# Optimization experiments

Measured on AMD Instinct MI355X. Metric: run time of the kernel, lower is better.

Reference implementation:

```python
import jax, jax.numpy as jnp
import numpy as np

M, N, K, D_IN = 200, 6, 25, 784
GAMMA, EPS = 0.5, 0.5
TOTAL = M * N


def setup_inputs() -> dict:
    key = jax.random.key(0)
    ks = jax.random.split(key, 8)
    B = 16384
    def lin(kk, shape, fan_in):
        bound = 1.0 / np.sqrt(fan_in)
        return jax.random.uniform(kk, shape, jnp.float32, -bound, bound)
    return {
        "batch_x": jax.random.normal(ks[0], (B, D_IN), jnp.float32),
        "Wa": lin(ks[1], (M, D_IN), D_IN),
        "ba": lin(ks[2], (M,), D_IN),
        "Wb": lin(ks[3], (TOTAL, TOTAL), TOTAL),
        "bb": lin(ks[4], (TOTAL,), TOTAL),
        "Wd": lin(ks[5], (D_IN, M), M),
        "bd": lin(ks[6], (D_IN,), M),
    }


def _step(params, carry, x):
    Wa, ba, Wb, bb, Wd, bd = params
    x_b, phi, psi = carry
    # sigma: per-group drive broadcast over cells + full recurrent term, shape (m, n)
    z_a = (Wa @ x + ba)[:, None]                      # (m, 1)
    z_b = (Wb @ x_b + bb).reshape(M, N)               # (m, n)
    sigma = z_a + z_b
    # inhibited activity
    pi = (1.0 - phi) * (sigma - sigma.min() + 1.0)    # (m, n)
    lambda_i = pi.max(axis=1)                         # (m,)
    # top-1 cell per group (scatter of topk indices == one-hot argmax)
    M_pi = jax.nn.one_hot(jnp.argmax(pi, axis=1), N, dtype=sigma.dtype)
    # top-k groups
    _, idx = jax.lax.top_k(lambda_i, K)
    M_lambda = jnp.zeros((M,), sigma.dtype).at[idx].set(1.0)[:, None]
    y = jnp.tanh(M_pi * M_lambda * sigma)             # (m, n)
    x_a_pred = Wd @ y.max(axis=1) + bd                # (D_in,)
    # memory / inhibition updates
    psi_n = jnp.maximum(EPS * psi, y)
    phi_n = jnp.maximum(GAMMA * phi, y)
    alpha = psi_n.sum()
    alpha = jnp.where(alpha == 0.0, 1.0, alpha)
    x_b_n = (psi_n / alpha).reshape(-1)
    # original detaches the recurrent state each step
    carry_n = (jax.lax.stop_gradient(x_b_n),
               jax.lax.stop_gradient(phi_n),
               jax.lax.stop_gradient(psi_n))
    return carry_n, x_a_pred


def reference(batch_x, Wa, ba, Wb, bb, Wd, bd):
    params = (Wa, ba, Wb, bb, Wd, bd)
    carry0 = (jnp.zeros((TOTAL,), batch_x.dtype),
              jnp.zeros((M, N), batch_x.dtype),
              jnp.zeros((M, N), batch_x.dtype))
    (x_b, phi, psi), preds = jax.lax.scan(
        lambda c, x: _step(params, c, x), carry0, batch_x)
    return preds, x_b, phi, psi
```

## Files before the change

### kernel.cpp

```cpp
#include <hip/hip_runtime.h>
#include <math.h>

#define Tn   16384
#define Mg   200
#define Nc   6
#define TOT  1200
#define Kk   25
#define Din  784
#define SP   28

__global__ void transpose_k(const float* __restrict__ src, float* __restrict__ dst,
                            int R, int C) {
    __shared__ float tile[32][33];
    int bx = blockIdx.x * 32, by = blockIdx.y * 32;
    int x = bx + threadIdx.x;
    for (int j = 0; j < 32; j += 8) {
        int y = by + threadIdx.y + j;
        if (x < C && y < R) tile[threadIdx.y + j][threadIdx.x] = src[(size_t)y * C + x];
    }
    __syncthreads();
    int x2 = by + threadIdx.x;
    for (int j = 0; j < 32; j += 8) {
        int y2 = bx + threadIdx.y + j;
        if (x2 < R && y2 < C) dst[(size_t)y2 * R + x2] = tile[threadIdx.x][threadIdx.y + j];
    }
}

__global__ void za_k(const float* __restrict__ X, const float* __restrict__ Wa,
                     const float* __restrict__ ba, float* __restrict__ Za) {
    __shared__ float xs[16][788];
    const int tid = threadIdx.x;
    const int t0  = blockIdx.x * 16;
    for (int idx = tid; idx < 16 * Din; idx += 256) {
        int tt = idx / Din, kk = idx - tt * Din;
        xs[tt][kk] = X[(size_t)(t0 + tt) * Din + kk];
    }
    __syncthreads();
    const int tq = tid & 15, gq = tid >> 4;
    const float4* xrow = reinterpret_cast<const float4*>(&xs[tq][0]);
    for (int g = gq; g < Mg; g += 16) {
        float acc = ba[g];
        const float4* wrow = reinterpret_cast<const float4*>(Wa + (size_t)g * Din);
        for (int k4 = 0; k4 < Din / 4; ++k4) {
            float4 a = xrow[k4], b = wrow[k4];
            acc = fmaf(a.x, b.x, acc); acc = fmaf(a.y, b.y, acc);
            acc = fmaf(a.z, b.z, acc); acc = fmaf(a.w, b.w, acc);
        }
        Za[(size_t)(t0 + tq) * Mg + g] = acc;
    }
}

__launch_bounds__(384, 1)
__global__ void serial_k(const float* __restrict__ Za, const float* __restrict__ WbT,
                         const float* __restrict__ bb,
                         unsigned long long* __restrict__ YP,
                         float* __restrict__ outTail) {
    __shared__ alignas(16) float sigma_sh[50 * SP];
    __shared__ alignas(16) float minp[8];
    __shared__ alignas(16) float selD[32];
    __shared__ alignas(16) int   selO[32];
    __shared__ float alphaS;

    const int tid  = threadIdx.x;
    const int lane = tid & 63;

    if (tid < 64) {
        const bool grp = (lane < 50);
        const int sgb  = lane * SP;
        const int cell0 = 24 * lane;
        const unsigned long long lt = (1ull << lane) - 1ull;

        float ps[24];
        #pragma unroll
        for (int i = 0; i < 24; ++i) ps[i] = 0.f;
        unsigned long long thw = 0ull;
        int slotr[4] = {-1, -1, -1, -1};
        unsigned long long yv64[4] = {0ull, 0ull, 0ull, 0ull};
        int bj[4] = {0, 0, 0, 0};
        float dcl[4] = {0.f, 0.f, 0.f, 0.f};

        __syncthreads();

        for (int t = 0; t < Tn; ++t) {
            if (t > 0) {
                #pragma unroll
                for (int c = 0; c < 4; ++c)
                    if (slotr[c] >= 0) YP[(size_t)(t - 1) * Kk + slotr[c]] = yv64[c];
            }

            float4 mp4 = *reinterpret_cast<const float4*>(minp);
            float m = fminf(fminf(fminf(mp4.x, mp4.y), fminf(mp4.z, mp4.w)), minp[4]);
            const float m1 = 1.f - m;

            float sg[24];
            if (grp) {
                #pragma unroll
                for (int q = 0; q < 6; ++q) {
                    float4 v = *reinterpret_cast<const float4*>(sigma_sh + sgb + 4 * q);
                    sg[4*q] = v.x; sg[4*q+1] = v.y; sg[4*q+2] = v.z; sg[4*q+3] = v.w;
                }
            } else {
                #pragma unroll
                for (int i = 0; i < 24; ++i) sg[i] = 0.f;
            }

            float bs[4], bp[4]; unsigned long long kb[4];
            #pragma unroll
            for (int c = 0; c < 4; ++c) { bs[c]=0.f; bp[c]=0.f; bj[c]=0; kb[c]=0ull; }
            if (grp) {
                #pragma unroll
                for (int c = 0; c < 4; ++c) {
                    float best = -INFINITY, sbv = 0.f, pbv = 0.f; int jb = 0;
                    #pragma unroll
                    for (int j = 0; j < 6; ++j) {
                        int i = 6 * c + j;
                        float pv = (1.f - ps[i]) * (sg[i] + m1);
                        bool bet = pv > best;
                        best = bet ? pv : best;
                        jb  = bet ? j : jb;
                        sbv = bet ? sg[i] : sbv;
                        pbv = bet ? ps[i] : pbv;
                    }
                    unsigned ub = __float_as_uint(best);
                    ub ^= (unsigned)(((int)ub) >> 31) | 0x80000000u;
                    int g = 4 * lane + c;
                    kb[c] = ((unsigned long long)ub << 32) |
                            (unsigned long long)(0xFFFFFFFFu - (unsigned)g);
                    bs[c] = sbv; bp[c] = pbv; bj[c] = jb;
                }
            }

            unsigned long long A = 0ull, B = ~0ull;
            unsigned long long p = thw;
            unsigned long long theta;
            while (true) {
                int cnt = __popcll(__ballot(kb[0] >= p)) + __popcll(__ballot(kb[1] >= p))
                        + __popcll(__ballot(kb[2] >= p)) + __popcll(__ballot(kb[3] >= p));
                if (cnt == Kk) { theta = p; break; }
                if (cnt > Kk) A = p; else B = p;
                unsigned long long m0 = __ballot(kb[0] > A && kb[0] < B);
                unsigned long long m1b = __ballot(kb[1] > A && kb[1] < B);
                unsigned long long m2 = __ballot(kb[2] > A && kb[2] < B);
                unsigned long long m3 = __ballot(kb[3] > A && kb[3] < B);
                int cls; unsigned long long mm;
                if (m0)       { cls = 0; mm = m0; }
                else if (m1b) { cls = 1; mm = m1b; }
                else if (m2)  { cls = 2; mm = m2; }
                else          { cls = 3; mm = m3; }
                int sl = __ffsll(mm) - 1;
                unsigned long long kc = (cls==0)?kb[0]:(cls==1)?kb[1]:(cls==2)?kb[2]:kb[3];
                p = __shfl(kc, sl);
            }
            thw = theta;

            unsigned long long M0 = __ballot(kb[0] >= theta);
            unsigned long long M1 = __ballot(kb[1] >= theta);
            unsigned long long M2 = __ballot(kb[2] >= theta);
            unsigned long long M3 = __ballot(kb[3] >= theta);
            int base1 = __popcll(M0);
            int base2 = base1 + __popcll(M1);
            int base3 = base2 + __popcll(M2);

            #pragma unroll
            for (int c = 0; c < 4; ++c) {
                slotr[c] = -1;
                unsigned long long Mc = (c==0)?M0:(c==1)?M1:(c==2)?M2:M3;
                int bse = (c==0)?0:(c==1)?base1:(c==2)?base2:base3;
                bool s = grp && (kb[c] >= theta);
                float d = 0.f;
                if (s) {
                    int slot = bse + __popcll(Mc & lt);
                    float x = fminf(fmaxf(bs[c], -9.f), 9.f);
                    float e = __expf(2.f * x);
                    float y = 1.f - 2.f / (e + 1.f);
                    float yv = fmaxf(y, 0.f);
                    d = fmaxf(y - 0.5f * bp[c], 0.f);
                    int g = 4 * lane + c;
                    selD[slot] = d;
                    selO[slot] = (6 * g + bj[c]) * TOT;
                    slotr[c] = slot;
                    yv64[c] = ((unsigned long long)(unsigned)g << 32) |
                              (unsigned long long)__float_as_uint(yv);
                }
                dcl[c] = d;
            }

            __syncthreads();

            if (grp) {
                #pragma unroll
                for (int c = 0; c < 4; ++c) {
                    #pragma unroll
                    for (int j = 0; j < 6; ++j) {
                        int i = 6 * c + j;
                        float add = (j == bj[c]) ? dcl[c] : 0.f;
                        ps[i] = fmaf(ps[i], 0.5f, add);
                    }
                }
            }

            __syncthreads();
        }

        #pragma unroll
        for (int c = 0; c < 4; ++c)
            if (slotr[c] >= 0) YP[(size_t)(Tn - 1) * Kk + slotr[c]] = yv64[c];
        if (grp) {
            float a = alphaS;
            float inv2 = (a == 0.f) ? 1.f : (1.f / a);
            #pragma unroll
            for (int i = 0; i < 24; ++i) {
                outTail[cell0 + i]           = ps[i] * inv2;
                outTail[TOT + cell0 + i]     = ps[i];
                outTail[2 * TOT + cell0 + i] = ps[i];
            }
        }
    } else {
        const int j = tid - 64;
        const bool act = (j < 300);
        const int w = (tid >> 6) - 1;
        const int base = act ? 4 * j : 0;
        const int saddr = act ? ((j / 6) * SP + (4 * j) % 24) : 0;
        const int g0 = base / 6, g1 = (base + 3) / 6;
        const bool f1 = ((base + 1) / 6) != g0;
        const bool f2 = ((base + 2) / 6) != g0;
        const bool f3 = ((base + 3) / 6) != g0;

        float4 cb4 = make_float4(0.f, 0.f, 0.f, 0.f);
        if (act) cb4 = *reinterpret_cast<const float4*>(bb + base);
        float4 uo = make_float4(0.f, 0.f, 0.f, 0.f);
        float alpha = 0.f;

        {
            float za0 = act ? Za[g0] : 0.f;
            float za1 = act ? Za[g1] : 0.f;
            float s0 = cb4.x + za0;
            float s1 = cb4.y + (f1 ? za1 : za0);
            float s2 = cb4.z + (f2 ? za1 : za0);
            float s3 = cb4.w + (f3 ? za1 : za0);
            if (act)
                *reinterpret_cast<float4*>(sigma_sh + saddr) = make_float4(s0,s1,s2,s3);
            float lm = act ? fminf(fminf(s0, s1), fminf(s2, s3)) : INFINITY;
            #pragma unroll
            for (int o = 1; o < 64; o <<= 1) lm = fminf(lm, __shfl_xor(lm, o));
            if (lane == 0) minp[w] = lm;
        }
        __syncthreads();

        for (int t = 0; t < Tn; ++t) {
            uo.x *= 0.5f; uo.y *= 0.5f; uo.z *= 0.5f; uo.w *= 0.5f;

            __syncthreads();

            float vD = 0.f; int vO = 0;
            if (lane < 25) { vD = selD[lane]; vO = selO[lane]; }

            const int tn = (t + 1 < Tn) ? t + 1 : t;
            float nza0 = act ? Za[(size_t)tn * Mg + g0] : 0.f;
            float nza1 = act ? Za[(size_t)tn * Mg + g1] : 0.f;
            float4 cc[Kk];
            #pragma unroll
            for (int k = 0; k < Kk; ++k) {
                int offk = __builtin_amdgcn_readlane(vO, k);
                cc[k] = *reinterpret_cast<const float4*>(WbT + offk + base);
            }
            __builtin_amdgcn_sched_barrier(0);

            float av = vD;
            #pragma unroll
            for (int o = 1; o < 64; o <<= 1) av += __shfl_xor(av, o);
            alpha = fmaf(alpha, 0.5f, av);
            const float A0  = (alpha == 0.f) ? 1.f : alpha;
            const float inv = 1.f / A0;
            if (w == 0 && lane == 0) alphaS = alpha;

            #pragma unroll
            for (int k = 0; k < Kk; ++k) {
                float dk = __uint_as_float(
                    (unsigned)__builtin_amdgcn_readlane((int)__float_as_uint(vD), k));
                uo.x = fmaf(dk, cc[k].x, uo.x);
                uo.y = fmaf(dk, cc[k].y, uo.y);
                uo.z = fmaf(dk, cc[k].z, uo.z);
                uo.w = fmaf(dk, cc[k].w, uo.w);
            }

            float s0 = fmaf(uo.x, inv, cb4.x + nza0);
            float s1 = fmaf(uo.y, inv, cb4.y + (f1 ? nza1 : nza0));
            float s2 = fmaf(uo.z, inv, cb4.z + (f2 ? nza1 : nza0));
            float s3 = fmaf(uo.w, inv, cb4.w + (f3 ? nza1 : nza0));
            if (act)
                *reinterpret_cast<float4*>(sigma_sh + saddr) = make_float4(s0,s1,s2,s3);
            float lm = act ? fminf(fminf(s0, s1), fminf(s2, s3)) : INFINITY;
            #pragma unroll
            for (int o = 1; o < 64; o <<= 1) lm = fminf(lm, __shfl_xor(lm, o));
            if (lane == 0) minp[w] = lm;

            __syncthreads();
        }
    }
}

__global__ void preds_k(const unsigned long long* __restrict__ YP,
                        const float* __restrict__ WdT, const float* __restrict__ bd,
                        float* __restrict__ out) {
    const int t = blockIdx.x;
    __shared__ float sv[Kk];
    __shared__ int   si[Kk];
    if (threadIdx.x < Kk) {
        unsigned long long v = YP[(size_t)t * Kk + threadIdx.x];
        sv[threadIdx.x] = __uint_as_float((unsigned)v);
        si[threadIdx.x] = (int)(v >> 32);
    }
    __syncthreads();
    for (int d = threadIdx.x; d < Din; d += 256) {
        float acc = bd[d];
        #pragma unroll
        for (int k = 0; k < Kk; ++k)
            acc = fmaf(sv[k], WdT[(size_t)si[k] * Din + d], acc);
        out[(size_t)t * Din + d] = acc;
    }
}

extern "C" void kernel_launch(void* const* d_in, const int* in_sizes, int n_in,
                              void* d_out, int out_size, void* d_ws, size_t ws_size,
                              hipStream_t stream) {
    const float* X  = (const float*)d_in[0];
    const float* Wa = (const float*)d_in[1];
    const float* ba = (const float*)d_in[2];
    const float* Wb = (const float*)d_in[3];
    const float* bb = (const float*)d_in[4];
    const float* Wd = (const float*)d_in[5];
    const float* bd = (const float*)d_in[6];
    float* out = (float*)d_out;

    float* w    = (float*)d_ws;
    float* Za   = w;
    float* WbT  = Za  + (size_t)Tn * Mg;
    float* WdT  = WbT + (size_t)TOT * TOT;
    unsigned long long* YP =
        (unsigned long long*)(WdT + (size_t)Mg * Din);

    dim3 tb(32, 8);
    transpose_k<<<dim3((TOT + 31) / 32, (TOT + 31) / 32), tb, 0, stream>>>(Wb, WbT, TOT, TOT);
    transpose_k<<<dim3((Mg + 31) / 32, (Din + 31) / 32), tb, 0, stream>>>(Wd, WdT, Din, Mg);
    za_k<<<Tn / 16, 256, 0, stream>>>(X, Wa, ba, Za);
    serial_k<<<1, 384, 0, stream>>>(Za, WbT, bb, YP, out + (size_t)Tn * Din);
    preds_k<<<Tn, 256, 0, stream>>>(YP, WdT, bd, out);
}
```

Baseline: 71.35 ms.

## Parallelize serial recurrence via speculative chunks with warmup and sequential repair

Splits the 16384-step recurrence into 128-step chunks, each run by its own block starting from zero state after a 160-step warmup. The bet is that the decaying state converges so the chunk's start state matches the true one. A single repair block then walks the chunks in order and compares the true carried state bitwise with each chunk's recorded start state. On a match it jumps to the chunk's end state; otherwise it re-runs that chunk serially. The cost is extra parallel work plus workspace reuse (WdT now aliases Sst), and if states rarely match bitwise the repair pass falls back to a fully serial run.

```diff
diff --git a/kernel.cpp b/kernel.cpp
--- a/kernel.cpp
+++ b/kernel.cpp
@@ -8,6 +8,10 @@
 #define Kk   25
 #define Din  784
 #define SP   28
+#define CHK  128
+#define WUP  160
+#define NCH  (Tn / CHK)
+#define STSZ 2404
 
 __global__ void transpose_k(const float* __restrict__ src, float* __restrict__ dst,
                             int R, int C) {
@@ -50,29 +54,21 @@
     }
 }
 
-__launch_bounds__(384, 1)
-__global__ void serial_k(const float* __restrict__ Za, const float* __restrict__ WbT,
-                         const float* __restrict__ bb,
-                         unsigned long long* __restrict__ YP,
-                         float* __restrict__ outTail) {
-    __shared__ alignas(16) float sigma_sh[50 * SP];
-    __shared__ alignas(16) float minp[8];
-    __shared__ alignas(16) float selD[32];
-    __shared__ alignas(16) int   selO[32];
-    __shared__ float alphaS;
-
+__device__ __forceinline__ void run_steps(
+    int tbeg, int treal, int tend,
+    const float* __restrict__ Za, const float* __restrict__ WbT,
+    const float* __restrict__ bb, unsigned long long* __restrict__ YP,
+    float* __restrict__ dS, float* __restrict__ dF,
+    float* sigma_sh, float* minp, float* selD, int* selO, float* alphaS,
+    float* ps, float4& uo, float& alpha)
+{
     const int tid  = threadIdx.x;
     const int lane = tid & 63;
 
     if (tid < 64) {
         const bool grp = (lane < 50);
         const int sgb  = lane * SP;
-        const int cell0 = 24 * lane;
         const unsigned long long lt = (1ull << lane) - 1ull;
-
-        float ps[24];
-        #pragma unroll
-        for (int i = 0; i < 24; ++i) ps[i] = 0.f;
         unsigned long long thw = 0ull;
         int slotr[4] = {-1, -1, -1, -1};
         unsigned long long yv64[4] = {0ull, 0ull, 0ull, 0ull};
@@ -81,8 +77,12 @@
 
         __syncthreads();
 
-        for (int t = 0; t < Tn; ++t) {
-            if (t > 0) {
+        for (int t = tbeg; t < tend; ++t) {
+            if (dS && t == treal && grp) {
+                #pragma unroll
+                for (int i = 0; i < 24; ++i) dS[24 * lane + i] = ps[i];
+            }
+            if (t - 1 >= treal) {
                 #pragma unroll
                 for (int c = 0; c < 4; ++c)
                     if (slotr[c] >= 0) YP[(size_t)(t - 1) * Kk + slotr[c]] = yv64[c];
@@ -204,16 +204,10 @@
 
         #pragma unroll
         for (int c = 0; c < 4; ++c)
-            if (slotr[c] >= 0) YP[(size_t)(Tn - 1) * Kk + slotr[c]] = yv64[c];
-        if (grp) {
-            float a = alphaS;
-            float inv2 = (a == 0.f) ? 1.f : (1.f / a);
-            #pragma unroll
-            for (int i = 0; i < 24; ++i) {
-                outTail[cell0 + i]           = ps[i] * inv2;
-                outTail[TOT + cell0 + i]     = ps[i];
-                outTail[2 * TOT + cell0 + i] = ps[i];
-            }
+            if (slotr[c] >= 0) YP[(size_t)(tend - 1) * Kk + slotr[c]] = yv64[c];
+        if (dF && grp) {
+            #pragma unroll
+            for (int i = 0; i < 24; ++i) dF[24 * lane + i] = ps[i];
         }
     } else {
         const int j = tid - 64;
@@ -228,16 +222,16 @@
 
         float4 cb4 = make_float4(0.f, 0.f, 0.f, 0.f);
         if (act) cb4 = *reinterpret_cast<const float4*>(bb + base);
-        float4 uo = make_float4(0.f, 0.f, 0.f, 0.f);
-        float alpha = 0.f;
 
         {
-            float za0 = act ? Za[g0] : 0.f;
-            float za1 = act ? Za[g1] : 0.f;
-            float s0 = cb4.x + za0;
-            float s1 = cb4.y + (f1 ? za1 : za0);
-            float s2 = cb4.z + (f2 ? za1 : za0);
-            float s3 = cb4.w + (f3 ? za1 : za0);
+            float za0 = act ? Za[(size_t)tbeg * Mg + g0] : 0.f;
+            float za1 = act ? Za[(size_t)tbeg * Mg + g1] : 0.f;
+            const float A0  = (alpha == 0.f) ? 1.f : alpha;
+            const float inv = 1.f / A0;
+            float s0 = fmaf(uo.x, inv, cb4.x + za0);
+            float s1 = fmaf(uo.y, inv, cb4.y + (f1 ? za1 : za0));
+            float s2 = fmaf(uo.z, inv, cb4.z + (f2 ? za1 : za0));
+            float s3 = fmaf(uo.w, inv, cb4.w + (f3 ? za1 : za0));
             if (act)
                 *reinterpret_cast<float4*>(sigma_sh + saddr) = make_float4(s0,s1,s2,s3);
             float lm = act ? fminf(fminf(s0, s1), fminf(s2, s3)) : INFINITY;
@@ -247,7 +241,11 @@
         }
         __syncthreads();
 
-        for (int t = 0; t < Tn; ++t) {
+        for (int t = tbeg; t < tend; ++t) {
+            if (dS && t == treal) {
+                if (act) *reinterpret_cast<float4*>(dS + 1200 + base) = uo;
+                if (tid == 64) dS[2400] = alpha;
+            }
             uo.x *= 0.5f; uo.y *= 0.5f; uo.z *= 0.5f; uo.w *= 0.5f;
 
             __syncthreads();
@@ -255,7 +253,7 @@
             float vD = 0.f; int vO = 0;
             if (lane < 25) { vD = selD[lane]; vO = selO[lane]; }
 
-            const int tn = (t + 1 < Tn) ? t + 1 : t;
+            const int tn = (t + 1 < tend) ? t + 1 : t;
             float nza0 = act ? Za[(size_t)tn * Mg + g0] : 0.f;
             float nza1 = act ? Za[(size_t)tn * Mg + g1] : 0.f;
             float4 cc[Kk];
@@ -272,7 +270,7 @@
             alpha = fmaf(alpha, 0.5f, av);
             const float A0  = (alpha == 0.f) ? 1.f : alpha;
             const float inv = 1.f / A0;
-            if (w == 0 && lane == 0) alphaS = alpha;
+            if (tid == 64) *alphaS = alpha;
 
             #pragma unroll
             for (int k = 0; k < Kk; ++k) {
@@ -296,6 +294,124 @@
             if (lane == 0) minp[w] = lm;
 
             __syncthreads();
+        }
+        if (dF) {
+            if (act) *reinterpret_cast<float4*>(dF + 1200 + base) = uo;
+            if (tid == 64) dF[2400] = alpha;
+        }
+    }
+}
+
+__launch_bounds__(384, 1)
+__global__ void chunk_k(const float* __restrict__ Za, const float* __restrict__ WbT,
+                        const float* __restrict__ bb,
+                        unsigned long long* __restrict__ YP,
+                        float* __restrict__ Sst, float* __restrict__ Fst) {
+    __shared__ alignas(16) float sigma_sh[50 * SP];
+    __shared__ alignas(16) float minp[8];
+    __shared__ alignas(16) float selD[32];
+    __shared__ alignas(16) int   selO[32];
+    __shared__ float alphaS;
+
+    const int chk = blockIdx.x;
+    const int treal = chk * CHK;
+    int tbeg = treal - WUP;
+    if (tbeg < 0) tbeg = 0;
+    const int tend  = treal + CHK;
+
+    float ps[24];
+    #pragma unroll
+    for (int i = 0; i < 24; ++i) ps[i] = 0.f;
+    float4 uo = make_float4(0.f, 0.f, 0.f, 0.f);
+    float alpha = 0.f;
+
+    run_steps(tbeg, treal, tend, Za, WbT, bb, YP,
+              Sst + (size_t)chk * STSZ, Fst + (size_t)chk * STSZ,
+              sigma_sh, minp, selD, selO, &alphaS, ps, uo, alpha);
+}
+
+__launch_bounds__(384, 1)
+__global__ void repair_k(const float* __restrict__ Za, const float* __restrict__ WbT,
+                         const float* __restrict__ bb,
+                         unsigned long long* __restrict__ YP,
+                         const float* __restrict__ Sst, const float* __restrict__ Fst,
+                         float* __restrict__ outTail) {
+    __shared__ alignas(16) float sigma_sh[50 * SP];
+    __shared__ alignas(16) float minp[8];
+    __shared__ alignas(16) float selD[32];
+    __shared__ alignas(16) int   selO[32];
+    __shared__ float alphaS;
+    __shared__ int okS;
+
+    const int tid  = threadIdx.x;
+    const int lane = tid & 63;
+
+    float ps[24];
+    #pragma unroll
+    for (int i = 0; i < 24; ++i) ps[i] = 0.f;
+    float4 uo = make_float4(0.f, 0.f, 0.f, 0.f);
+    float alpha = 0.f;
+
+    for (int c = 0; c < NCH; ++c) {
+        if (tid == 0) okS = 1;
+        __syncthreads();
+
+        const float* S = Sst + (size_t)c * STSZ;
+        int ok = 1;
+        if (tid < 64) {
+            if (lane < 50) {
+                #pragma unroll
+                for (int i = 0; i < 24; ++i)
+                    ok &= (__float_as_uint(ps[i]) == __float_as_uint(S[24 * lane + i]));
+            }
+        } else {
+            const int j = tid - 64;
+            if (j < 300) {
+                const float* up = S + 1200 + 4 * j;
+                ok &= (__float_as_uint(uo.x) == __float_as_uint(up[0]));
+                ok &= (__float_as_uint(uo.y) == __float_as_uint(up[1]));
+                ok &= (__float_as_uint(uo.z) == __float_as_uint(up[2]));
+                ok &= (__float_as_uint(uo.w) == __float_as_uint(up[3]));
+            }
+            if (tid == 64)
+                ok &= (__float_as_uint(alpha) == __float_as_uint(S[2400]));
+        }
+        if (!ok) okS = 0;
+        __syncthreads();
+        const int good = okS;
+        __syncthreads();
+
+        if (good) {
+            const float* F = Fst + (size_t)c * STSZ;
+            if (tid < 64) {
+                if (lane < 50) {
+                    #pragma unroll
+                    for (int i = 0; i < 24; ++i) ps[i] = F[24 * lane + i];
+                }
+            } else {
+                const int j = tid - 64;
+                if (j < 300) uo = *reinterpret_cast<const float4*>(F + 1200 + 4 * j);
+                alpha = F[2400];
+            }
+        } else {
+            run_steps(c * CHK, c * CHK, (c + 1) * CHK, Za, WbT, bb, YP,
+                      nullptr, nullptr, sigma_sh, minp, selD, selO, &alphaS,
+                      ps, uo, alpha);
+        }
+    }
+
+    __syncthreads();
+    if (tid == 64) alphaS = alpha;
+    __syncthreads();
+    if (tid < 64 && lane < 50) {
+        const int cell0 = 24 * lane;
+        float a = alphaS;
+        float inv2 = (a == 0.f) ? 1.f : (1.f / a);
+        #pragma unroll
+        for (int i = 0; i < 24; ++i) {
+            outTail[cell0 + i]           = ps[i] * inv2;
+            outTail[TOT + cell0 + i]     = ps[i];
+            outTail[2 * TOT + cell0 + i] = ps[i];
         }
     }
 }
@@ -336,14 +452,17 @@
     float* w    = (float*)d_ws;
     float* Za   = w;
     float* WbT  = Za  + (size_t)Tn * Mg;
-    float* WdT  = WbT + (size_t)TOT * TOT;
     unsigned long long* YP =
-        (unsigned long long*)(WdT + (size_t)Mg * Din);
+        (unsigned long long*)(WbT + (size_t)TOT * TOT);
+    float* Sst  = (float*)(YP + (size_t)Tn * Kk);
+    float* Fst  = Sst + (size_t)NCH * STSZ;
+    float* WdT  = Sst;
 
     dim3 tb(32, 8);
     transpose_k<<<dim3((TOT + 31) / 32, (TOT + 31) / 32), tb, 0, stream>>>(Wb, WbT, TOT, TOT);
+    za_k<<<Tn / 16, 256, 0, stream>>>(X, Wa, ba, Za);
+    chunk_k<<<NCH, 384, 0, stream>>>(Za, WbT, bb, YP, Sst, Fst);
+    repair_k<<<1, 384, 0, stream>>>(Za, WbT, bb, YP, Sst, Fst, out + (size_t)Tn * Din);
     transpose_k<<<dim3((Mg + 31) / 32, (Din + 31) / 32), tb, 0, stream>>>(Wd, WdT, Din, Mg);
-    za_k<<<Tn / 16, 256, 0, stream>>>(X, Wa, ba, Za);
-    serial_k<<<1, 384, 0, stream>>>(Za, WbT, bb, YP, out + (size_t)Tn * Din);
     preds_k<<<Tn, 256, 0, stream>>>(YP, WdT, bd, out);
 }
```

After: 75.85 ms. 1.06x slower.
